# Optimization experiments

Hardware: AMD Instinct MI355X
Metric: run time of the kernel (lower is better)

## Reference

```python
import jax, jax.numpy as jnp
import numpy as np

SEQ, D_IN, D_H, D_OUT = 8192, 1024, 2048, 1024


def setup_inputs() -> dict:
    key = jax.random.key(0)
    ks = jax.random.split(key, 5)
    # small init scales keep tanh out of full saturation (torch code uses randn,
    # but unit-scale weights would saturate; math is identical regardless of scale)
    return {
        "x_seq": jax.random.normal(ks[0], (SEQ, D_IN), jnp.float32),
        "h0": jnp.zeros((D_H,), jnp.float32),
        "W_ih": jax.random.normal(ks[1], (D_H, D_IN), jnp.float32) / np.sqrt(D_IN),
        "W_hh": jax.random.normal(ks[2], (D_H, D_H), jnp.float32) / np.sqrt(D_H),
        "b_h": jnp.zeros((D_H,), jnp.float32),
        "W_ho_w": jax.random.normal(ks[3], (D_OUT, D_H), jnp.float32) / np.sqrt(D_H),
        "W_ho_b": jnp.zeros((D_OUT,), jnp.float32),
    }


def reference(x_seq, h0, W_ih, W_hh, b_h, W_ho_w, W_ho_b):
    # Precompute the input projection for all steps at once (same math as
    # W_ih @ x_t per step, just batched): (S, H)
    xw = x_seq @ W_ih.T + b_h

    def step(h, xw_t):
        h = jnp.tanh(xw_t + W_hh @ h)  # recurrent matvec + tanh
        return h, h

    h_final, hs = jax.lax.scan(step, h0, xw)  # hs: (S, H)
    outputs = hs @ W_ho_w.T + W_ho_b          # (S, O)
    return outputs, h_final
```

## Files before the change

kernel.cpp:

```cpp
#include <hip/hip_runtime.h>
#include <hip/hip_bf16.h>

#define SEQ   8192
#define DIN   1024
#define DH    2048
#define DOUT  1024

#define SENT 0x7fc0deadu

__global__ __launch_bounds__(256) void fill_sent_kernel(uint4* __restrict__ p, size_t n4) {
    size_t i = (size_t)blockIdx.x * blockDim.x + threadIdx.x;
    size_t stride = (size_t)gridDim.x * blockDim.x;
    uint4 v = make_uint4(SENT, SENT, SENT, SENT);
    for (; i < n4; i += stride) p[i] = v;
}

__global__ __launch_bounds__(256) void gemm_nt_bias(
    const float* __restrict__ A, const float* __restrict__ B,
    const float* __restrict__ bias, float* __restrict__ C,
    int M, int N, int K) {
    __shared__ float As[16][132];
    __shared__ float Bs[16][68];
    const int tid = threadIdx.x;
    const int bm = blockIdx.x * 128;
    const int bn = blockIdx.y * 64;
    const int alr = tid >> 1;
    const int alk = (tid & 1) * 8;
    const int blr = tid >> 2;
    const int blk = (tid & 3) * 4;
    const int tm = (tid >> 4) * 8;
    const int tn = (tid & 15) * 4;
    float acc[8][4] = {};

    for (int k0 = 0; k0 < K; k0 += 16) {
        const float4 a0 = *(const float4*)&A[(size_t)(bm + alr) * K + k0 + alk];
        const float4 a1 = *(const float4*)&A[(size_t)(bm + alr) * K + k0 + alk + 4];
        const float4 bv = *(const float4*)&B[(size_t)(bn + blr) * K + k0 + blk];
        As[alk + 0][alr] = a0.x; As[alk + 1][alr] = a0.y;
        As[alk + 2][alr] = a0.z; As[alk + 3][alr] = a0.w;
        As[alk + 4][alr] = a1.x; As[alk + 5][alr] = a1.y;
        As[alk + 6][alr] = a1.z; As[alk + 7][alr] = a1.w;
        Bs[blk + 0][blr] = bv.x; Bs[blk + 1][blr] = bv.y;
        Bs[blk + 2][blr] = bv.z; Bs[blk + 3][blr] = bv.w;
        __syncthreads();
#pragma unroll
        for (int k = 0; k < 16; ++k) {
            const float4 af0 = *(const float4*)&As[k][tm];
            const float4 af1 = *(const float4*)&As[k][tm + 4];
            const float4 bf  = *(const float4*)&Bs[k][tn];
            const float a[8] = {af0.x, af0.y, af0.z, af0.w,
                                af1.x, af1.y, af1.z, af1.w};
            const float b[4] = {bf.x, bf.y, bf.z, bf.w};
#pragma unroll
            for (int i = 0; i < 8; ++i)
#pragma unroll
                for (int j = 0; j < 4; ++j)
                    acc[i][j] = fmaf(a[i], b[j], acc[i][j]);
        }
        __syncthreads();
    }

    const float4 bv = *(const float4*)&bias[bn + tn];
#pragma unroll
    for (int i = 0; i < 8; ++i) {
        float4 o;
        o.x = acc[i][0] + bv.x;
        o.y = acc[i][1] + bv.y;
        o.z = acc[i][2] + bv.z;
        o.w = acc[i][3] + bv.w;
        *(float4*)&C[(size_t)(bm + tm + i) * N + bn + tn] = o;
    }
}

__global__ __attribute__((amdgpu_flat_work_group_size(512, 512),
                          amdgpu_waves_per_eu(2, 2)))
void rnn_recurrence(
    const float* __restrict__ Whh, const float* __restrict__ xw,
    const float* __restrict__ h0, float* __restrict__ hs) {
    __shared__ float part[2][8][16];
    const int tid = threadIdx.x;
    const int wave = tid >> 6;
    const int lane = tid & 63;
    const int rbase = blockIdx.x * 16;
    const int c0 = 4 * tid;

    float4 w[16];
#pragma unroll
    for (int r = 0; r < 16; ++r) {
        w[r] = *(const float4*)&Whh[(size_t)(rbase + r) * DH + c0];
        asm volatile("" : "+v"(w[r].x), "+v"(w[r].y), "+v"(w[r].z), "+v"(w[r].w));
    }

    for (int t = 0; t < SEQ; ++t) {
        const int par = t & 1;
        float xwv = 0.f;
        if (tid < 16) xwv = xw[(size_t)t * DH + rbase + tid];

        float4 hv;
        if (t == 0) {
            hv = *(const float4*)&h0[c0];
        } else {
            const float* a0 = hs + (size_t)(t - 1) * DH + c0;
            unsigned bad;
            do {
                asm volatile(
                    "global_load_dwordx4 %0, %1, off sc0 sc1\n\t"
                    "s_waitcnt vmcnt(0)"
                    : "=&v"(hv) : "v"(a0) : "memory");
                bad = (__float_as_uint(hv.x) == SENT) | (__float_as_uint(hv.y) == SENT) |
                      (__float_as_uint(hv.z) == SENT) | (__float_as_uint(hv.w) == SENT);
            } while (__builtin_expect(bad != 0, 0));
        }

        float acc[16];
#pragma unroll
        for (int r = 0; r < 16; ++r)
            acc[r] = fmaf(w[r].w, hv.w,
                     fmaf(w[r].z, hv.z,
                     fmaf(w[r].y, hv.y, w[r].x * hv.x)));

        const bool b0 = (lane & 1) != 0, b1 = (lane & 2) != 0,
                   b2 = (lane & 4) != 0, b3 = (lane & 8) != 0;
        float s8[8];
#pragma unroll
        for (int j = 0; j < 8; ++j) {
            const float k = b0 ? acc[2 * j + 1] : acc[2 * j];
            const float g = b0 ? acc[2 * j]     : acc[2 * j + 1];
            s8[j] = k + __shfl_xor(g, 1);
        }
        float s4[4];
#pragma unroll
        for (int j = 0; j < 4; ++j) {
            const float k = b1 ? s8[2 * j + 1] : s8[2 * j];
            const float g = b1 ? s8[2 * j]     : s8[2 * j + 1];
            s4[j] = k + __shfl_xor(g, 2);
        }
        float s2[2];
#pragma unroll
        for (int j = 0; j < 2; ++j) {
            const float k = b2 ? s4[2 * j + 1] : s4[2 * j];
            const float g = b2 ? s4[2 * j]     : s4[2 * j + 1];
            s2[j] = k + __shfl_xor(g, 4);
        }
        float s1;
        {
            const float k = b3 ? s2[1] : s2[0];
            const float g = b3 ? s2[0] : s2[1];
            s1 = k + __shfl_xor(g, 8);
        }
        s1 += __shfl_xor(s1, 16);
        s1 += __shfl_xor(s1, 32);

        if (lane < 16) part[par][wave][lane] = s1;
        __syncthreads();

        if (tid < 16) {
            const float sum =
                part[par][0][tid] + part[par][1][tid] + part[par][2][tid] +
                part[par][3][tid] + part[par][4][tid] + part[par][5][tid] +
                part[par][6][tid] + part[par][7][tid];
            const float hval = tanhf(sum + xwv);
            __hip_atomic_store((unsigned*)(hs + (size_t)t * DH + rbase + tid),
                               __float_as_uint(hval),
                               __ATOMIC_RELAXED, __HIP_MEMORY_SCOPE_AGENT);
        }
    }
}

__global__ __launch_bounds__(256) void copy_hfinal(const float* __restrict__ hs,
                                                   float* __restrict__ out) {
    const int i = blockIdx.x * 256 + threadIdx.x;
    out[i] = hs[(size_t)(SEQ - 1) * DH + i];
}

extern "C" void kernel_launch(void* const* d_in, const int* in_sizes, int n_in,
                              void* d_out, int out_size, void* d_ws, size_t ws_size,
                              hipStream_t stream) {
    (void)in_sizes; (void)n_in; (void)out_size; (void)ws_size;
    const float* x_seq  = (const float*)d_in[0];
    const float* h0     = (const float*)d_in[1];
    const float* W_ih   = (const float*)d_in[2];
    const float* W_hh   = (const float*)d_in[3];
    const float* b_h    = (const float*)d_in[4];
    const float* W_ho_w = (const float*)d_in[5];
    const float* W_ho_b = (const float*)d_in[6];
    float* out = (float*)d_out;

    float* xw = (float*)d_ws;
    float* hs = xw + (size_t)SEQ * DH;

    fill_sent_kernel<<<2048, 256, 0, stream>>>((uint4*)hs, (size_t)SEQ * DH / 4);

    gemm_nt_bias<<<dim3(SEQ / 128, DH / 64), 256, 0, stream>>>(
        x_seq, W_ih, b_h, xw, SEQ, DH, DIN);

    rnn_recurrence<<<DH / 16, 512, 0, stream>>>(W_hh, xw, h0, hs);

    gemm_nt_bias<<<dim3(SEQ / 128, DOUT / 64), 256, 0, stream>>>(
        hs, W_ho_w, W_ho_b, out, SEQ, DOUT, DH);

    copy_hfinal<<<DH / 256, 256, 0, stream>>>(hs, out + (size_t)SEQ * DOUT);
}
```

Measured before the change: 14.57 ms.

## Use bf16 MFMA for the output projection GEMM

```diff
diff --git a/kernel.cpp b/kernel.cpp
--- a/kernel.cpp
+++ b/kernel.cpp
@@ -7,12 +7,32 @@
 #define DOUT  1024
 
 #define SENT 0x7fc0deadu
+
+typedef __attribute__((ext_vector_type(8))) short bf16frag;
+typedef __attribute__((ext_vector_type(4))) float f32x4;
 
 __global__ __launch_bounds__(256) void fill_sent_kernel(uint4* __restrict__ p, size_t n4) {
     size_t i = (size_t)blockIdx.x * blockDim.x + threadIdx.x;
     size_t stride = (size_t)gridDim.x * blockDim.x;
     uint4 v = make_uint4(SENT, SENT, SENT, SENT);
     for (; i < n4; i += stride) p[i] = v;
+}
+
+static __device__ inline unsigned short f2bf(float f) {
+    unsigned u = __float_as_uint(f);
+    u += 0x7fffu + ((u >> 16) & 1u);
+    return (unsigned short)(u >> 16);
+}
+__global__ __launch_bounds__(256) void cvt_bf16_kernel(
+    const float4* __restrict__ src, ushort4* __restrict__ dst, size_t n4) {
+    size_t i = (size_t)blockIdx.x * blockDim.x + threadIdx.x;
+    size_t stride = (size_t)gridDim.x * blockDim.x;
+    for (; i < n4; i += stride) {
+        const float4 v = src[i];
+        ushort4 o;
+        o.x = f2bf(v.x); o.y = f2bf(v.y); o.z = f2bf(v.z); o.w = f2bf(v.w);
+        dst[i] = o;
+    }
 }
 
 __global__ __launch_bounds__(256) void gemm_nt_bias(
@@ -72,6 +92,42 @@
     }
 }
 
+__global__ __launch_bounds__(256) void gemm_bf16_mfma(
+    const unsigned short* __restrict__ A, const unsigned short* __restrict__ B,
+    const float* __restrict__ bias, float* __restrict__ C,
+    int M, int N, int K) {
+    const int tid = threadIdx.x;
+    const int wave = tid >> 6;
+    const int lane = tid & 63;
+    const int bm = blockIdx.x * 64 + wave * 16;
+    const int bn = blockIdx.y * 64;
+    const int r  = lane & 15;
+    const int ks = (lane >> 4) * 8;
+
+    f32x4 acc[4] = {};
+    const unsigned short* arow = A + (size_t)(bm + r) * K + ks;
+    const unsigned short* brow = B + (size_t)(bn + r) * K + ks;
+
+    for (int k0 = 0; k0 < K; k0 += 32) {
+        const bf16frag a = *(const bf16frag*)(arow + k0);
+#pragma unroll
+        for (int ct = 0; ct < 4; ++ct) {
+            const bf16frag b = *(const bf16frag*)(brow + (size_t)ct * 16 * K + k0);
+            acc[ct] = __builtin_amdgcn_mfma_f32_16x16x32_bf16(a, b, acc[ct], 0, 0, 0);
+        }
+    }
+
+    const int orow = bm + (lane >> 4) * 4;
+#pragma unroll
+    for (int ct = 0; ct < 4; ++ct) {
+        const int col = bn + ct * 16 + (lane & 15);
+        const float bv = bias[col];
+#pragma unroll
+        for (int i = 0; i < 4; ++i)
+            C[(size_t)(orow + i) * N + col] = acc[ct][i] + bv;
+    }
+}
+
 __global__ __attribute__((amdgpu_flat_work_group_size(512, 512),
                           amdgpu_waves_per_eu(2, 2)))
 void rnn_recurrence(
@@ -188,6 +244,8 @@
 
     float* xw = (float*)d_ws;
     float* hs = xw + (size_t)SEQ * DH;
+    unsigned short* hsb = (unsigned short*)xw;
+    unsigned short* wob = hsb + (size_t)SEQ * DH;
 
     fill_sent_kernel<<<2048, 256, 0, stream>>>((uint4*)hs, (size_t)SEQ * DH / 4);
 
@@ -196,8 +254,13 @@
 
     rnn_recurrence<<<DH / 16, 512, 0, stream>>>(W_hh, xw, h0, hs);
 
-    gemm_nt_bias<<<dim3(SEQ / 128, DOUT / 64), 256, 0, stream>>>(
-        hs, W_ho_w, W_ho_b, out, SEQ, DOUT, DH);
+    cvt_bf16_kernel<<<2048, 256, 0, stream>>>(
+        (const float4*)hs, (ushort4*)hsb, (size_t)SEQ * DH / 4);
+    cvt_bf16_kernel<<<1024, 256, 0, stream>>>(
+        (const float4*)W_ho_w, (ushort4*)wob, (size_t)DOUT * DH / 4);
+
+    gemm_bf16_mfma<<<dim3(SEQ / 64, DOUT / 64), 256, 0, stream>>>(
+        hsb, wob, W_ho_b, out, SEQ, DOUT, DH);
 
     copy_hfinal<<<DH / 256, 256, 0, stream>>>(hs, out + (size_t)SEQ * DOUT);
 }
```

After: 14.38 ms. No clear change (-1.3%).
